# Optimization experiments

Measured on AMD Instinct MI355X. Metric: run time of the kernel, lower is better.

The kernel has to match this reference:

```python
import jax, jax.numpy as jnp
import numpy as np

B, N, D, C = 4, 8192, 256, 1000
EPS = 1e-5


def expmap0(x, c=-1.0, eps=EPS):
    # Poincare-ball exponential map at the origin (matches torch version).
    x_norm = jnp.maximum(jnp.linalg.norm(x, axis=-1, keepdims=True), eps)
    curve_norm = jnp.sqrt(-c) * x_norm
    scale = jnp.tanh(curve_norm) / curve_norm
    return scale * x


def setup_inputs() -> dict:
    key = jax.random.key(0)
    k1, k2, k3 = jax.random.split(key, 3)
    features = jax.random.normal(k1, (B, N, D), dtype=jnp.float32)
    # kaiming-uniform-like scale for a 256-fan-in linear / embedding table
    lim = 1.0 / np.sqrt(D)
    W = jax.random.uniform(k2, (D, D), dtype=jnp.float32, minval=-lim, maxval=lim)
    b = jnp.zeros((D,), dtype=jnp.float32)
    embeddings = jax.random.uniform(k3, (C, D), dtype=jnp.float32, minval=-lim, maxval=lim)
    logit_scale = jnp.zeros((), dtype=jnp.float32)  # log(1.0)
    return {"features": features, "W": W, "b": b,
            "embeddings": embeddings, "logit_scale": logit_scale}


def reference(features, W, b, embeddings, logit_scale):
    # projection (nn.Linear): y = x @ W^T + b
    x = jnp.einsum("bnd,ed->bne", features, W) + b
    # map features and prototypes onto the Poincare ball (curvature = -1)
    x = expmap0(x)                       # [B, N, D], norms < 1
    protos = expmap0(embeddings)         # [C, D],    norms < 1

    # pairwise Poincare distance, computed via the norm expansion
    x_sq = jnp.sum(x * x, axis=-1)               # [B, N]
    p_sq = jnp.sum(protos * protos, axis=-1)     # [C]
    xp = jnp.einsum("bnd,cd->bnc", x, protos)    # [B, N, C]
    diff_sq = jnp.maximum(x_sq[..., None] + p_sq[None, None, :] - 2.0 * xp, 0.0)

    denom = jnp.maximum((1.0 - x_sq)[..., None] * (1.0 - p_sq)[None, None, :], EPS)
    argument = jnp.maximum(1.0 + 2.0 * diff_sq / denom, 1.0 + EPS)
    dists = jnp.arccosh(argument)                # [B, N, C]

    scale = jnp.minimum(jnp.exp(logit_scale), 100.0)
    return -dists * scale
```

## Files before the change

kernel.cpp:

```cpp
#include <hip/hip_runtime.h>
#include <hip/hip_fp16.h>


#define EPSF 1e-5f

typedef _Float16 half8 __attribute__((ext_vector_type(8)));
typedef _Float16 half4v __attribute__((ext_vector_type(4)));
typedef float f32x4 __attribute__((ext_vector_type(4)));

typedef __attribute__((address_space(3))) unsigned int as3_u32;
typedef __attribute__((address_space(1))) unsigned int as1_u32;
#define GLOAD16(gp, lp) __builtin_amdgcn_global_load_lds(  \
    (const as1_u32*)(gp), (as3_u32*)(lp), 16, 0, 0)

static __device__ __forceinline__ f32x4 mfma16(half8 a, half8 b, f32x4 c) {
  return __builtin_amdgcn_mfma_f32_16x16x32_f16(a, b, c, 0, 0, 0);
}

#define PROTO_OFF 0
#define PSQ_OFF   (1024 * 512)
#define WIMG_OFF  (1024 * 512 + 4096)
#define WS_BYTES  (WIMG_OFF + 2 * 65536)

#define LDS_SZ (65536 + 65536 + 512 + 1024)

__global__ __launch_bounds__(256) void prep_kernel(const float* __restrict__ W,
                                                   const float* __restrict__ emb,
                                                   char* __restrict__ ws) {
  const int blk = blockIdx.x;
  const int tid = threadIdx.x;
  if (blk < 256) {
    const int wave = tid >> 6, lane = tid & 63;
    const int row = blk * 4 + wave;
    float4 v = {0.f, 0.f, 0.f, 0.f};
    if (row < 1000) v = ((const float4*)emb)[row * 64 + lane];
    float s = v.x * v.x + v.y * v.y + v.z * v.z + v.w * v.w;
#pragma unroll
    for (int m = 1; m < 64; m <<= 1) s += __shfl_xor(s, m, 64);
    float r  = sqrtf(s);
    float rc = fmaxf(r, EPSF);
    float e  = __expf(2.0f * rc);
    float t  = 1.0f - 2.0f / (e + 1.0f);
    float sc = t / rc;
    float ps = t * t;
    if (row >= 1000) { sc = 0.0f; ps = 0.0f; }
    half4v h;
    h[0] = (_Float16)(v.x * sc); h[1] = (_Float16)(v.y * sc);
    h[2] = (_Float16)(v.z * sc); h[3] = (_Float16)(v.w * sc);
    const int byte = (lane * 8) ^ ((row & 7) << 4);
    *(half4v*)(ws + PROTO_OFF + row * 512 + byte) = h;
    if (lane == 0) ((float*)(ws + PSQ_OFF))[row] = ps;
  } else {
    const int e4 = (blk - 256) * 256 + tid;
    const int n  = e4 >> 6;
    const int k4 = e4 & 63;
    const int k  = k4 * 4;
    float4 v = ((const float4*)W)[n * 64 + k4];
    const int c  = k >> 7;
    const int kl = k & 127;
    half4v h;
    h[0] = (_Float16)v.x; h[1] = (_Float16)v.y;
    h[2] = (_Float16)v.z; h[3] = (_Float16)v.w;
    const int byte = (kl * 2) ^ ((n & 7) << 4);
    *(half4v*)(ws + WIMG_OFF + c * 65536 + n * 256 + byte) = h;
  }
}

__global__ __launch_bounds__(256, 1) void main_kernel(
    const float* __restrict__ fea, const float* __restrict__ bvec,
    const float* __restrict__ lsc, const char* __restrict__ ws,
    float* __restrict__ out) {
  extern __shared__ char lds[];
  char* regA = lds;
  char* regB = lds + 65536;
  float* xsq = (float*)(lds + 131072);
  float* bl  = (float*)(lds + 131072 + 512);

  const int tid  = threadIdx.x;
  const int wave = tid >> 6, lane = tid & 63;
  const int g = lane >> 4, i = lane & 15;
  const int m0 = blockIdx.x * 128;
  const int xr = (i & 7) << 4;

  const char*  wimg  = ws + WIMG_OFF;
  const char*  pimg  = ws + PROTO_OFF;
  const float* psq_g = (const float*)(ws + PSQ_OFF);

  for (int j = wave; j < 64; j += 4) GLOAD16(wimg + j * 1024 + lane * 16, regB + j * 1024);
  bl[tid] = bvec[tid];
#pragma unroll
  for (int j = 0; j < 16; ++j) {
    const int u = j * 256 + tid;
    const int row = u >> 5, c8 = u & 31;
    const float4* p = (const float4*)fea + (size_t)(m0 + row) * 64 + c8 * 2;
    float4 a = p[0], b4 = p[1];
    half8 h = {(_Float16)a.x,  (_Float16)a.y,  (_Float16)a.z,  (_Float16)a.w,
               (_Float16)b4.x, (_Float16)b4.y, (_Float16)b4.z, (_Float16)b4.w};
    *(half8*)(regA + row * 512 + ((c8 * 16) ^ ((row & 7) << 4))) = h;
  }
  __syncthreads();

  f32x4 accP[2][16];
  const f32x4 zero4 = {0.f, 0.f, 0.f, 0.f};
#pragma unroll
  for (int rf = 0; rf < 2; ++rf)
#pragma unroll
    for (int cf = 0; cf < 16; ++cf) accP[rf][cf] = zero4;

#pragma unroll
  for (int c = 0; c < 2; ++c) {
    if (c == 1) {
      __syncthreads();
      for (int j = wave; j < 64; j += 4) GLOAD16(wimg + 65536 + j * 1024 + lane * 16, regB + j * 1024);
      __syncthreads();
    }
#pragma unroll
    for (int ks = 0; ks < 4; ++ks) {
      const int kb  = ks * 64 + g * 16;
      const int kbA = c * 256 + kb;
      half8 a0 = *(half8*)(regA + (wave * 32 + 0 + i) * 512 + (kbA ^ xr));
      half8 a1 = *(half8*)(regA + (wave * 32 + 16 + i) * 512 + (kbA ^ xr));
#pragma unroll
      for (int cf = 0; cf < 16; ++cf) {
        half8 b8 = *(half8*)(regB + (cf * 16 + i) * 256 + (kb ^ xr));
        accP[0][cf] = mfma16(a0, b8, accP[0][cf]);
        accP[1][cf] = mfma16(a1, b8, accP[1][cf]);
      }
    }
  }

  float ssum[2][4] = {{0.f,0.f,0.f,0.f},{0.f,0.f,0.f,0.f}};
#pragma unroll
  for (int rf = 0; rf < 2; ++rf)
#pragma unroll
    for (int cf = 0; cf < 16; ++cf) {
      const float bc = bl[i + 16 * cf];
#pragma unroll
      for (int reg = 0; reg < 4; ++reg) {
        accP[rf][cf][reg] += bc;
        ssum[rf][reg] = fmaf(accP[rf][cf][reg], accP[rf][cf][reg], ssum[rf][reg]);
      }
    }
#pragma unroll
  for (int m = 1; m < 16; m <<= 1)
#pragma unroll
    for (int rf = 0; rf < 2; ++rf)
#pragma unroll
      for (int reg = 0; reg < 4; ++reg) ssum[rf][reg] += __shfl_xor(ssum[rf][reg], m, 64);

  float scl[2][4], xsv[2][4];
#pragma unroll
  for (int rf = 0; rf < 2; ++rf)
#pragma unroll
    for (int reg = 0; reg < 4; ++reg) {
      float r  = sqrtf(ssum[rf][reg]);
      float rc = fmaxf(r, EPSF);
      float e  = __expf(2.0f * rc);
      float t  = 1.0f - 2.0f / (e + 1.0f);
      scl[rf][reg] = t / rc;
      xsv[rf][reg] = t * t;
    }
  __syncthreads();

#pragma unroll
  for (int rf = 0; rf < 2; ++rf)
#pragma unroll
    for (int cf = 0; cf < 16; ++cf)
#pragma unroll
      for (int reg = 0; reg < 4; ++reg) {
        const int row = wave * 32 + rf * 16 + g * 4 + reg;
        const int col = i + 16 * cf;
        *(_Float16*)(regB + row * 512 + ((col * 2) ^ ((row & 7) << 4))) =
            (_Float16)(accP[rf][cf][reg] * scl[rf][reg]);
      }
  if (i < 8) {
    const int rf = i >> 2, reg = i & 3;
    xsq[wave * 32 + rf * 16 + g * 4 + reg] = xsv[rf][reg];
  }
  for (int j = wave; j < 64; j += 4) GLOAD16(pimg + j * 1024 + lane * 16, regA + j * 1024);
  __syncthreads();

  const int wr = (wave >> 1) * 64, wc = (wave & 1) * 64;
  const float sc_out = fminf(__expf(lsc[0]), 100.0f);
  float xs_l[4][4];
#pragma unroll
  for (int rf = 0; rf < 4; ++rf)
#pragma unroll
    for (int reg = 0; reg < 4; ++reg) xs_l[rf][reg] = xsq[wr + rf * 16 + g * 4 + reg];

  for (int nt = 0; nt < 8; ++nt) {
    f32x4 acc[4][4];
#pragma unroll
    for (int rf = 0; rf < 4; ++rf)
#pragma unroll
      for (int cf = 0; cf < 4; ++cf) acc[rf][cf] = zero4;

#pragma unroll
    for (int ks = 0; ks < 8; ++ks) {
      const int kb = ks * 64 + g * 16;
      half8 A[4], B[4];
#pragma unroll
      for (int rf = 0; rf < 4; ++rf) A[rf] = *(half8*)(regB + (wr + rf * 16 + i) * 512 + (kb ^ xr));
#pragma unroll
      for (int cf = 0; cf < 4; ++cf) B[cf] = *(half8*)(regA + (wc + cf * 16 + i) * 512 + (kb ^ xr));
#pragma unroll
      for (int rf = 0; rf < 4; ++rf)
#pragma unroll
        for (int cf = 0; cf < 4; ++cf) acc[rf][cf] = mfma16(A[rf], B[cf], acc[rf][cf]);
    }
    __syncthreads();
    if (nt < 7)
      for (int j = wave; j < 64; j += 4)
        GLOAD16(pimg + (size_t)(nt + 1) * 65536 + j * 1024 + lane * 16, regA + j * 1024);

#pragma unroll
    for (int cf = 0; cf < 4; ++cf) {
      const int col = nt * 128 + wc + cf * 16 + i;
      const bool ok = col < 1000;
      const float ps  = ok ? psq_g[col] : 0.0f;
      const float omp = 1.0f - ps;
#pragma unroll
      for (int rf = 0; rf < 4; ++rf)
#pragma unroll
        for (int reg = 0; reg < 4; ++reg) {
          const float xs   = xs_l[rf][reg];
          const float dot  = acc[rf][cf][reg];
          const float diff = fmaxf(fmaf(-2.0f, dot, xs + ps), 0.0f);
          const float den  = fmaxf((1.0f - xs) * omp, EPSF);
          const float arg  = fmaxf(fmaf(2.0f * diff, __builtin_amdgcn_rcpf(den), 1.0f),
                                   1.0f + EPSF);
          const float sq   = __builtin_amdgcn_sqrtf(fmaf(arg, arg, -1.0f));
          const float dist = __logf(arg + sq);
          if (ok)
            out[(size_t)(m0 + wr + rf * 16 + g * 4 + reg) * 1000 + col] = -dist * sc_out;
        }
    }
    if (nt < 7) __syncthreads();
  }
}

__global__ __launch_bounds__(256) void fallback_kernel(
    const float* __restrict__ fea, const float* __restrict__ W,
    const float* __restrict__ b, const float* __restrict__ emb,
    const float* __restrict__ lsc, float* __restrict__ out) {
  __shared__ float fr_[16][256];
  __shared__ float xr_[16][256];
  __shared__ float xs_[16];
  const int tid  = threadIdx.x;
  const int row0 = blockIdx.x * 16;

  for (int u = tid; u < 16 * 256; u += 256)
    fr_[u >> 8][u & 255] = fea[(size_t)(row0 + (u >> 8)) * 256 + (u & 255)];
  __syncthreads();

  float acc[16];
  const float bj = b[tid];
#pragma unroll
  for (int r = 0; r < 16; ++r) acc[r] = bj;
  for (int k = 0; k < 256; ++k) {
    const float w = W[(size_t)tid * 256 + k];
#pragma unroll
    for (int r = 0; r < 16; ++r) acc[r] = fmaf(fr_[r][k], w, acc[r]);
  }
#pragma unroll
  for (int r = 0; r < 16; ++r) xr_[r][tid] = acc[r];
  __syncthreads();

  if (tid < 16) {
    float s = 0.f;
    for (int k = 0; k < 256; ++k) s = fmaf(xr_[tid][k], xr_[tid][k], s);
    const float rn = sqrtf(s), rc = fmaxf(rn, EPSF);
    const float e = __expf(2.f * rc), t = 1.f - 2.f / (e + 1.f);
    xs_[tid] = t * t;
    fr_[tid][0] = t / rc;
  }
  __syncthreads();
  for (int u = tid; u < 16 * 256; u += 256)
    xr_[u >> 8][u & 255] *= fr_[u >> 8][0];
  __syncthreads();

  const float sc_out = fminf(__expf(lsc[0]), 100.0f);
  for (int c = tid; c < 1000; c += 256) {
    float s = 0.f;
    for (int k = 0; k < 256; ++k) {
      const float e0 = emb[(size_t)c * 256 + k];
      s = fmaf(e0, e0, s);
    }
    const float rn = sqrtf(s), rc = fmaxf(rn, EPSF);
    const float e = __expf(2.f * rc), t = 1.f - 2.f / (e + 1.f);
    const float psc = t / rc, ps = t * t, omp = 1.f - ps;
    float dots[16];
#pragma unroll
    for (int r = 0; r < 16; ++r) dots[r] = 0.f;
    for (int k = 0; k < 256; ++k) {
      const float pk = emb[(size_t)c * 256 + k] * psc;
#pragma unroll
      for (int r = 0; r < 16; ++r) dots[r] = fmaf(xr_[r][k], pk, dots[r]);
    }
#pragma unroll
    for (int r = 0; r < 16; ++r) {
      const float xs = xs_[r];
      const float diff = fmaxf(xs + ps - 2.f * dots[r], 0.f);
      const float den  = fmaxf((1.f - xs) * omp, EPSF);
      const float arg  = fmaxf(1.f + 2.f * diff / den, 1.f + EPSF);
      const float d    = logf(arg + sqrtf(fmaf(arg, arg, -1.f)));
      out[(size_t)(row0 + r) * 1000 + c] = -d * sc_out;
    }
  }
}

extern "C" void kernel_launch(void* const* d_in, const int* in_sizes, int n_in,
                              void* d_out, int out_size, void* d_ws, size_t ws_size,
                              hipStream_t stream) {
  (void)in_sizes; (void)n_in; (void)out_size;
  const float* fea = (const float*)d_in[0];
  const float* W   = (const float*)d_in[1];
  const float* b   = (const float*)d_in[2];
  const float* emb = (const float*)d_in[3];
  const float* ls  = (const float*)d_in[4];
  float* out = (float*)d_out;
  char*  ws  = (char*)d_ws;

  if (ws_size >= (size_t)WS_BYTES) {
    hipFuncSetAttribute((const void*)main_kernel,
                        hipFuncAttributeMaxDynamicSharedMemorySize, LDS_SZ);
    prep_kernel<<<320, 256, 0, stream>>>(W, emb, ws);
    main_kernel<<<256, 256, LDS_SZ, stream>>>(fea, b, ls, ws, out);
  } else {
    fallback_kernel<<<2048, 256, 0, stream>>>(fea, W, b, emb, ls, out);
  }
}
```

Measured before the change: 210.1 us.

## Restructure fused kernel to 64-row tiles with 64KB LDS and double-buffered prototypes

Replaces the 128-row, 130KB-LDS main kernel with a 64-row-per-block kernel using 64KB static LDS and two blocks per CU, launched as 512 blocks. W is now converted to fp16 inside the kernel in four double-buffered K-chunks instead of in the prep kernel. Features are loaded straight into registers. Each wave owns 16 rows and keeps its A fragments in registers across 16 double-buffered prototype tiles synchronised with explicit waitcnt and barriers. The log is switched to log2 with ln2 folded into the output scale. The aim is better occupancy and overlap of prototype loads with MFMA and epilogue work. The cost is redundant W conversion in every block and more manual synchronisation.

```diff
diff --git a/kernel.cpp b/kernel.cpp
--- a/kernel.cpp
+++ b/kernel.cpp
@@ -19,223 +19,190 @@
 
 #define PROTO_OFF 0
 #define PSQ_OFF   (1024 * 512)
-#define WIMG_OFF  (1024 * 512 + 4096)
-#define WS_BYTES  (WIMG_OFF + 2 * 65536)
-
-#define LDS_SZ (65536 + 65536 + 512 + 1024)
-
-__global__ __launch_bounds__(256) void prep_kernel(const float* __restrict__ W,
-                                                   const float* __restrict__ emb,
+#define WS_BYTES  (PSQ_OFF + 4096)
+
+__global__ __launch_bounds__(256) void prep_kernel(const float* __restrict__ emb,
                                                    char* __restrict__ ws) {
-  const int blk = blockIdx.x;
   const int tid = threadIdx.x;
-  if (blk < 256) {
-    const int wave = tid >> 6, lane = tid & 63;
-    const int row = blk * 4 + wave;
-    float4 v = {0.f, 0.f, 0.f, 0.f};
-    if (row < 1000) v = ((const float4*)emb)[row * 64 + lane];
-    float s = v.x * v.x + v.y * v.y + v.z * v.z + v.w * v.w;
-#pragma unroll
-    for (int m = 1; m < 64; m <<= 1) s += __shfl_xor(s, m, 64);
-    float r  = sqrtf(s);
-    float rc = fmaxf(r, EPSF);
+  const int wave = tid >> 6, lane = tid & 63;
+  const int row = blockIdx.x * 4 + wave;
+  float4 v = {0.f, 0.f, 0.f, 0.f};
+  if (row < 1000) v = ((const float4*)emb)[row * 64 + lane];
+  float s = v.x * v.x + v.y * v.y + v.z * v.z + v.w * v.w;
+#pragma unroll
+  for (int m = 1; m < 64; m <<= 1) s += __shfl_xor(s, m, 64);
+  float r  = sqrtf(s);
+  float rc = fmaxf(r, EPSF);
+  float e  = __expf(2.0f * rc);
+  float t  = 1.0f - 2.0f / (e + 1.0f);
+  float sc = t / rc;
+  float ps = t * t;
+  if (row >= 1000) { sc = 0.0f; ps = 0.0f; }
+  half4v h;
+  h[0] = (_Float16)(v.x * sc); h[1] = (_Float16)(v.y * sc);
+  h[2] = (_Float16)(v.z * sc); h[3] = (_Float16)(v.w * sc);
+  const int byte = (lane * 8) ^ ((row & 7) << 4);
+  *(half4v*)(ws + PROTO_OFF + row * 512 + byte) = h;
+  if (lane == 0) ((float*)(ws + PSQ_OFF))[row] = ps;
+}
+
+__global__ __launch_bounds__(256, 2) void fused_kernel(
+    const float* __restrict__ fea, const float* __restrict__ W,
+    const float* __restrict__ bvec, const float* __restrict__ lsc,
+    const char* __restrict__ ws, float* __restrict__ out) {
+  __shared__ char lds[65536];
+  char* buf0 = lds;
+  char* buf1 = lds + 32768;
+
+  const int tid  = threadIdx.x;
+  const int w    = tid >> 6, lane = tid & 63;
+  const int g = lane >> 4, i = lane & 15;
+  const int xr = (i & 7) << 4;
+  const int m0 = blockIdx.x * 64;
+
+  const char*  pimg  = ws + PROTO_OFF;
+  const float* psq_g = (const float*)(ws + PSQ_OFF);
+
+  const f32x4 z4 = {0.f, 0.f, 0.f, 0.f};
+  f32x4 accW[16];
+#pragma unroll
+  for (int cf = 0; cf < 16; ++cf) accW[cf] = z4;
+
+  auto stageW = [&](int c, char* dst) {
+#pragma unroll
+    for (int p = 0; p < 8; ++p) {
+      const int u = p * 256 + tid;
+      const int n = u >> 3, k8 = u & 7;
+      const float4* src = (const float4*)(W + (size_t)n * 256 + c * 64 + k8 * 8);
+      float4 v0 = src[0], v1 = src[1];
+      half8 h = {(_Float16)v0.x, (_Float16)v0.y, (_Float16)v0.z, (_Float16)v0.w,
+                 (_Float16)v1.x, (_Float16)v1.y, (_Float16)v1.z, (_Float16)v1.w};
+      *(half8*)(dst + n * 128 + ((k8 * 16) ^ ((n & 7) << 4))) = h;
+    }
+  };
+  auto mfmaW = [&](int c, const char* bsrc) {
+#pragma unroll
+    for (int ksl = 0; ksl < 2; ++ksl) {
+      const float4* ap = (const float4*)(fea +
+          (size_t)(m0 + w * 16 + i) * 256 + c * 64 + ksl * 32 + g * 8);
+      float4 a0 = ap[0], a1 = ap[1];
+      half8 a = {(_Float16)a0.x, (_Float16)a0.y, (_Float16)a0.z, (_Float16)a0.w,
+                 (_Float16)a1.x, (_Float16)a1.y, (_Float16)a1.z, (_Float16)a1.w};
+#pragma unroll
+      for (int cf = 0; cf < 16; ++cf) {
+        half8 b = *(const half8*)(bsrc + (cf * 16 + i) * 128 +
+                                  ((ksl * 64 + g * 16) ^ xr));
+        accW[cf] = mfma16(a, b, accW[cf]);
+      }
+    }
+  };
+
+  stageW(0, buf0); __syncthreads();
+  stageW(1, buf1); mfmaW(0, buf0); __syncthreads();
+  stageW(2, buf0); mfmaW(1, buf1); __syncthreads();
+  stageW(3, buf1); mfmaW(2, buf0); __syncthreads();
+  mfmaW(3, buf1);  __syncthreads();
+
+  auto stageP = [&](int nt, char* dst) {
+#pragma unroll
+    for (int p = 0; p < 8; ++p) {
+      const int chunk = p * 4 + w;
+      GLOAD16(pimg + (size_t)nt * 32768 + chunk * 1024 + lane * 16,
+              dst + chunk * 1024);
+    }
+  };
+  stageP(0, buf1);
+
+  float ssum[4] = {0.f, 0.f, 0.f, 0.f};
+#pragma unroll
+  for (int cf = 0; cf < 16; ++cf) {
+    const float bc = bvec[cf * 16 + i];
+#pragma unroll
+    for (int r = 0; r < 4; ++r) {
+      accW[cf][r] += bc;
+      ssum[r] = fmaf(accW[cf][r], accW[cf][r], ssum[r]);
+    }
+  }
+#pragma unroll
+  for (int m = 1; m < 16; m <<= 1)
+#pragma unroll
+    for (int r = 0; r < 4; ++r) ssum[r] += __shfl_xor(ssum[r], m, 64);
+
+  float scl[4], xsv[4];
+#pragma unroll
+  for (int r = 0; r < 4; ++r) {
+    float rn = sqrtf(ssum[r]);
+    float rc = fmaxf(rn, EPSF);
     float e  = __expf(2.0f * rc);
     float t  = 1.0f - 2.0f / (e + 1.0f);
-    float sc = t / rc;
-    float ps = t * t;
-    if (row >= 1000) { sc = 0.0f; ps = 0.0f; }
-    half4v h;
-    h[0] = (_Float16)(v.x * sc); h[1] = (_Float16)(v.y * sc);
-    h[2] = (_Float16)(v.z * sc); h[3] = (_Float16)(v.w * sc);
-    const int byte = (lane * 8) ^ ((row & 7) << 4);
-    *(half4v*)(ws + PROTO_OFF + row * 512 + byte) = h;
-    if (lane == 0) ((float*)(ws + PSQ_OFF))[row] = ps;
-  } else {
-    const int e4 = (blk - 256) * 256 + tid;
-    const int n  = e4 >> 6;
-    const int k4 = e4 & 63;
-    const int k  = k4 * 4;
-    float4 v = ((const float4*)W)[n * 64 + k4];
-    const int c  = k >> 7;
-    const int kl = k & 127;
-    half4v h;
-    h[0] = (_Float16)v.x; h[1] = (_Float16)v.y;
-    h[2] = (_Float16)v.z; h[3] = (_Float16)v.w;
-    const int byte = (kl * 2) ^ ((n & 7) << 4);
-    *(half4v*)(ws + WIMG_OFF + c * 65536 + n * 256 + byte) = h;
-  }
-}
-
-__global__ __launch_bounds__(256, 1) void main_kernel(
-    const float* __restrict__ fea, const float* __restrict__ bvec,
-    const float* __restrict__ lsc, const char* __restrict__ ws,
-    float* __restrict__ out) {
-  extern __shared__ char lds[];
-  char* regA = lds;
-  char* regB = lds + 65536;
-  float* xsq = (float*)(lds + 131072);
-  float* bl  = (float*)(lds + 131072 + 512);
-
-  const int tid  = threadIdx.x;
-  const int wave = tid >> 6, lane = tid & 63;
-  const int g = lane >> 4, i = lane & 15;
-  const int m0 = blockIdx.x * 128;
-  const int xr = (i & 7) << 4;
-
-  const char*  wimg  = ws + WIMG_OFF;
-  const char*  pimg  = ws + PROTO_OFF;
-  const float* psq_g = (const float*)(ws + PSQ_OFF);
-
-  for (int j = wave; j < 64; j += 4) GLOAD16(wimg + j * 1024 + lane * 16, regB + j * 1024);
-  bl[tid] = bvec[tid];
-#pragma unroll
-  for (int j = 0; j < 16; ++j) {
-    const int u = j * 256 + tid;
-    const int row = u >> 5, c8 = u & 31;
-    const float4* p = (const float4*)fea + (size_t)(m0 + row) * 64 + c8 * 2;
-    float4 a = p[0], b4 = p[1];
-    half8 h = {(_Float16)a.x,  (_Float16)a.y,  (_Float16)a.z,  (_Float16)a.w,
-               (_Float16)b4.x, (_Float16)b4.y, (_Float16)b4.z, (_Float16)b4.w};
-    *(half8*)(regA + row * 512 + ((c8 * 16) ^ ((row & 7) << 4))) = h;
-  }
-  __syncthreads();
-
-  f32x4 accP[2][16];
-  const f32x4 zero4 = {0.f, 0.f, 0.f, 0.f};
-#pragma unroll
-  for (int rf = 0; rf < 2; ++rf)
-#pragma unroll
-    for (int cf = 0; cf < 16; ++cf) accP[rf][cf] = zero4;
-
-#pragma unroll
-  for (int c = 0; c < 2; ++c) {
-    if (c == 1) {
-      __syncthreads();
-      for (int j = wave; j < 64; j += 4) GLOAD16(wimg + 65536 + j * 1024 + lane * 16, regB + j * 1024);
-      __syncthreads();
-    }
-#pragma unroll
-    for (int ks = 0; ks < 4; ++ks) {
-      const int kb  = ks * 64 + g * 16;
-      const int kbA = c * 256 + kb;
-      half8 a0 = *(half8*)(regA + (wave * 32 + 0 + i) * 512 + (kbA ^ xr));
-      half8 a1 = *(half8*)(regA + (wave * 32 + 16 + i) * 512 + (kbA ^ xr));
-#pragma unroll
-      for (int cf = 0; cf < 16; ++cf) {
-        half8 b8 = *(half8*)(regB + (cf * 16 + i) * 256 + (kb ^ xr));
-        accP[0][cf] = mfma16(a0, b8, accP[0][cf]);
-        accP[1][cf] = mfma16(a1, b8, accP[1][cf]);
+    scl[r] = t / rc;
+    xsv[r] = t * t;
+  }
+
+  char* xsl = buf0 + w * 8192;
+#pragma unroll
+  for (int cf = 0; cf < 16; ++cf)
+#pragma unroll
+    for (int r = 0; r < 4; ++r) {
+      const int row = g * 4 + r;
+      *(_Float16*)(xsl + row * 512 + (((cf * 16 + i) * 2) ^ ((row & 7) << 4))) =
+          (_Float16)(accW[cf][r] * scl[r]);
+    }
+  half8 A[8];
+#pragma unroll
+  for (int ks = 0; ks < 8; ++ks)
+    A[ks] = *(const half8*)(xsl + i * 512 + ((ks * 64 + g * 16) ^ xr));
+
+  const float sc_ln2 = fminf(__expf(lsc[0]), 100.0f) * 0.69314718055994531f;
+
+  asm volatile("s_waitcnt vmcnt(0) lgkmcnt(0)" ::: "memory");
+  __builtin_amdgcn_s_barrier();
+  __builtin_amdgcn_sched_barrier(0);
+
+  auto stepP = [&](int nt, const char* cur, char* nxt) {
+    float psq[4];
+#pragma unroll
+    for (int cf = 0; cf < 4; ++cf) psq[cf] = psq_g[nt * 64 + cf * 16 + i];
+
+    if (nt < 15) stageP(nt + 1, nxt);
+
+    f32x4 acc[4] = {z4, z4, z4, z4};
+#pragma unroll
+    for (int ks = 0; ks < 8; ++ks) {
+#pragma unroll
+      for (int cf = 0; cf < 4; ++cf) {
+        half8 b = *(const half8*)(cur + (cf * 16 + i) * 512 +
+                                  ((ks * 64 + g * 16) ^ xr));
+        acc[cf] = mfma16(A[ks], b, acc[cf]);
       }
     }
-  }
-
-  float ssum[2][4] = {{0.f,0.f,0.f,0.f},{0.f,0.f,0.f,0.f}};
-#pragma unroll
-  for (int rf = 0; rf < 2; ++rf)
-#pragma unroll
-    for (int cf = 0; cf < 16; ++cf) {
-      const float bc = bl[i + 16 * cf];
-#pragma unroll
-      for (int reg = 0; reg < 4; ++reg) {
-        accP[rf][cf][reg] += bc;
-        ssum[rf][reg] = fmaf(accP[rf][cf][reg], accP[rf][cf][reg], ssum[rf][reg]);
+#pragma unroll
+    for (int cf = 0; cf < 4; ++cf) {
+      const float ps = psq[cf], omp = 1.0f - ps;
+      const int col = nt * 64 + cf * 16 + i;
+#pragma unroll
+      for (int r = 0; r < 4; ++r) {
+        const float xs   = xsv[r];
+        const float diff = fmaxf(fmaf(-2.0f, acc[cf][r], xs + ps), 0.0f);
+        const float den  = fmaxf((1.0f - xs) * omp, EPSF);
+        const float arg  = fmaxf(fmaf(2.0f * diff, __builtin_amdgcn_rcpf(den), 1.0f),
+                                 1.0f + EPSF);
+        const float sq   = __builtin_amdgcn_sqrtf(fmaf(arg, arg, -1.0f));
+        const float dist = __log2f(arg + sq);
+        if (col < 1000)
+          out[(size_t)(m0 + w * 16 + g * 4 + r) * 1000 + col] = -dist * sc_ln2;
       }
     }
-#pragma unroll
-  for (int m = 1; m < 16; m <<= 1)
-#pragma unroll
-    for (int rf = 0; rf < 2; ++rf)
-#pragma unroll
-      for (int reg = 0; reg < 4; ++reg) ssum[rf][reg] += __shfl_xor(ssum[rf][reg], m, 64);
-
-  float scl[2][4], xsv[2][4];
-#pragma unroll
-  for (int rf = 0; rf < 2; ++rf)
-#pragma unroll
-    for (int reg = 0; reg < 4; ++reg) {
-      float r  = sqrtf(ssum[rf][reg]);
-      float rc = fmaxf(r, EPSF);
-      float e  = __expf(2.0f * rc);
-      float t  = 1.0f - 2.0f / (e + 1.0f);
-      scl[rf][reg] = t / rc;
-      xsv[rf][reg] = t * t;
-    }
-  __syncthreads();
-
-#pragma unroll
-  for (int rf = 0; rf < 2; ++rf)
-#pragma unroll
-    for (int cf = 0; cf < 16; ++cf)
-#pragma unroll
-      for (int reg = 0; reg < 4; ++reg) {
-        const int row = wave * 32 + rf * 16 + g * 4 + reg;
-        const int col = i + 16 * cf;
-        *(_Float16*)(regB + row * 512 + ((col * 2) ^ ((row & 7) << 4))) =
-            (_Float16)(accP[rf][cf][reg] * scl[rf][reg]);
-      }
-  if (i < 8) {
-    const int rf = i >> 2, reg = i & 3;
-    xsq[wave * 32 + rf * 16 + g * 4 + reg] = xsv[rf][reg];
-  }
-  for (int j = wave; j < 64; j += 4) GLOAD16(pimg + j * 1024 + lane * 16, regA + j * 1024);
-  __syncthreads();
-
-  const int wr = (wave >> 1) * 64, wc = (wave & 1) * 64;
-  const float sc_out = fminf(__expf(lsc[0]), 100.0f);
-  float xs_l[4][4];
-#pragma unroll
-  for (int rf = 0; rf < 4; ++rf)
-#pragma unroll
-    for (int reg = 0; reg < 4; ++reg) xs_l[rf][reg] = xsq[wr + rf * 16 + g * 4 + reg];
-
-  for (int nt = 0; nt < 8; ++nt) {
-    f32x4 acc[4][4];
-#pragma unroll
-    for (int rf = 0; rf < 4; ++rf)
-#pragma unroll
-      for (int cf = 0; cf < 4; ++cf) acc[rf][cf] = zero4;
-
-#pragma unroll
-    for (int ks = 0; ks < 8; ++ks) {
-      const int kb = ks * 64 + g * 16;
-      half8 A[4], B[4];
-#pragma unroll
-      for (int rf = 0; rf < 4; ++rf) A[rf] = *(half8*)(regB + (wr + rf * 16 + i) * 512 + (kb ^ xr));
-#pragma unroll
-      for (int cf = 0; cf < 4; ++cf) B[cf] = *(half8*)(regA + (wc + cf * 16 + i) * 512 + (kb ^ xr));
-#pragma unroll
-      for (int rf = 0; rf < 4; ++rf)
-#pragma unroll
-        for (int cf = 0; cf < 4; ++cf) acc[rf][cf] = mfma16(A[rf], B[cf], acc[rf][cf]);
-    }
-    __syncthreads();
-    if (nt < 7)
-      for (int j = wave; j < 64; j += 4)
-        GLOAD16(pimg + (size_t)(nt + 1) * 65536 + j * 1024 + lane * 16, regA + j * 1024);
-
-#pragma unroll
-    for (int cf = 0; cf < 4; ++cf) {
-      const int col = nt * 128 + wc + cf * 16 + i;
-      const bool ok = col < 1000;
-      const float ps  = ok ? psq_g[col] : 0.0f;
-      const float omp = 1.0f - ps;
-#pragma unroll
-      for (int rf = 0; rf < 4; ++rf)
-#pragma unroll
-        for (int reg = 0; reg < 4; ++reg) {
-          const float xs   = xs_l[rf][reg];
-          const float dot  = acc[rf][cf][reg];
-          const float diff = fmaxf(fmaf(-2.0f, dot, xs + ps), 0.0f);
-          const float den  = fmaxf((1.0f - xs) * omp, EPSF);
-          const float arg  = fmaxf(fmaf(2.0f * diff, __builtin_amdgcn_rcpf(den), 1.0f),
-                                   1.0f + EPSF);
-          const float sq   = __builtin_amdgcn_sqrtf(fmaf(arg, arg, -1.0f));
-          const float dist = __logf(arg + sq);
-          if (ok)
-            out[(size_t)(m0 + wr + rf * 16 + g * 4 + reg) * 1000 + col] = -dist * sc_out;
-        }
-    }
-    if (nt < 7) __syncthreads();
+    if (nt < 15) {
+      asm volatile("s_waitcnt vmcnt(16)" ::: "memory");
+      __builtin_amdgcn_s_barrier();
+      __builtin_amdgcn_sched_barrier(0);
+    }
+  };
+
+  for (int nt2 = 0; nt2 < 16; nt2 += 2) {
+    stepP(nt2,     buf1, buf0);
+    stepP(nt2 + 1, buf0, buf1);
   }
 }
 
@@ -258,9 +225,9 @@
 #pragma unroll
   for (int r = 0; r < 16; ++r) acc[r] = bj;
   for (int k = 0; k < 256; ++k) {
-    const float w = W[(size_t)tid * 256 + k];
-#pragma unroll
-    for (int r = 0; r < 16; ++r) acc[r] = fmaf(fr_[r][k], w, acc[r]);
+    const float wv = W[(size_t)tid * 256 + k];
+#pragma unroll
+    for (int r = 0; r < 16; ++r) acc[r] = fmaf(fr_[r][k], wv, acc[r]);
   }
 #pragma unroll
   for (int r = 0; r < 16; ++r) xr_[r][tid] = acc[r];
@@ -322,10 +289,8 @@
   char*  ws  = (char*)d_ws;
 
   if (ws_size >= (size_t)WS_BYTES) {
-    hipFuncSetAttribute((const void*)main_kernel,
-                        hipFuncAttributeMaxDynamicSharedMemorySize, LDS_SZ);
-    prep_kernel<<<320, 256, 0, stream>>>(W, emb, ws);
-    main_kernel<<<256, 256, LDS_SZ, stream>>>(fea, b, ls, ws, out);
+    prep_kernel<<<256, 256, 0, stream>>>(emb, ws);
+    fused_kernel<<<512, 256, 0, stream>>>(fea, W, b, ls, ws, out);
   } else {
     fallback_kernel<<<2048, 256, 0, stream>>>(fea, W, b, emb, ls, out);
   }
```

After: 190.2 us. -9.5%, faster.
